# Optimization experiments

Measured on AMD Instinct MI355X. Metric: run time of the kernel, lower is better.

The kernel has to match this reference:

```python
import jax, jax.numpy as jnp
import numpy as np

N, E = 50000, 300000
IN, HID, OUT, HEADS = 768, 256, 128, 8
RELS = ("writes", "written_by", "cites")


def setup_inputs():
    ks = iter(jax.random.split(jax.random.key(0), 64))

    def nrm(shape, scale=1.0):
        return jax.random.normal(next(ks), shape, dtype=jnp.float32) * scale

    inp = {"x_paper": nrm((N, IN)), "x_author": nrm((N, IN))}
    for name in ("ei_writes", "ei_written_by", "ei_cites"):
        inp[name] = jax.random.randint(next(ks), (2, E), 0, N, dtype=jnp.int32)
    # layer 0: in=IN, out=HID, heads=HEADS
    s0 = 1.0 / np.sqrt(IN)
    inp["W0_paper"] = nrm((IN, HID), s0); inp["b0_paper"] = jnp.zeros((HID,), jnp.float32)
    inp["W0_author"] = nrm((IN, HID), s0); inp["b0_author"] = jnp.zeros((HID,), jnp.float32)
    D0 = HID // HEADS
    for rel in RELS:
        inp["a0s_" + rel] = nrm((HEADS, D0), 0.1)
        inp["a0d_" + rel] = nrm((HEADS, D0), 0.1)
    inp["Wk0"] = nrm((HID, HID), 1.0 / np.sqrt(HID)); inp["bk0"] = jnp.zeros((HID,), jnp.float32)
    inp["q0"] = nrm((HID,), 0.1)
    # layer 1 (last): in=HID, out=OUT, heads=1
    s1 = 1.0 / np.sqrt(HID)
    inp["W1_paper"] = nrm((HID, OUT), s1); inp["b1_paper"] = jnp.zeros((OUT,), jnp.float32)
    inp["W1_author"] = nrm((HID, OUT), s1); inp["b1_author"] = jnp.zeros((OUT,), jnp.float32)
    for rel in RELS:
        inp["a1s_" + rel] = nrm((1, OUT), 0.1)
        inp["a1d_" + rel] = nrm((1, OUT), 0.1)
    inp["Wk1"] = nrm((OUT, OUT), 1.0 / np.sqrt(OUT)); inp["bk1"] = jnp.zeros((OUT,), jnp.float32)
    inp["q1"] = nrm((OUT,), 0.1)
    return inp


def _han_layer(xs, proj, att, Wk, bk, q, edges, heads):
    # xs: {ntype: [N, in]}, proj: {ntype: (W, b)}, att: {rel: (a_src[H,D], a_dst[H,D])}
    C = q.shape[0]
    D = C // heads
    xh = {nt: (x @ proj[nt][0] + proj[nt][1]).reshape(-1, heads, D) for nt, x in xs.items()}
    outs = {nt: [] for nt in xs}
    for (st, rel, dt), ei in edges:
        a_s, a_d = att[rel]
        xsrc, xdst = xh[st], xh[dt]
        src, dst = ei[0], ei[1]
        n = xdst.shape[0]
        # GAT-style edge scores per head: [E, H]
        al = jax.nn.leaky_relu((xsrc * a_s).sum(-1)[src] + (xdst * a_d).sum(-1)[dst], 0.2)
        amax = jax.lax.stop_gradient(jax.ops.segment_max(al, dst, num_segments=n))
        ex = jnp.exp(al - amax[dst])
        alpha = ex / (jax.ops.segment_sum(ex, dst, num_segments=n)[dst] + 1e-16)
        msg = xsrc[src] * alpha[:, :, None]                      # [E, H, D]
        agg = jax.ops.segment_sum(msg, dst, num_segments=n)      # [n, H, D]
        outs[dt].append(jax.nn.relu(agg.reshape(n, C)))
    # semantic attention across metapaths (group)
    res = {}
    for nt, lst in outs.items():
        stk = jnp.stack(lst)                                     # [M, n, C]
        score = (q * jnp.tanh(stk @ Wk + bk).mean(axis=1)).sum(-1)
        w = jax.nn.softmax(score)                                # [M]
        res[nt] = jnp.einsum('m,mnc->nc', w, stk)
    return res


def reference(x_paper, x_author, W0_paper, b0_paper, W0_author, b0_author,
              a0s_writes, a0d_writes, a0s_written_by, a0d_written_by, a0s_cites, a0d_cites,
              Wk0, bk0, q0,
              W1_paper, b1_paper, W1_author, b1_author,
              a1s_writes, a1d_writes, a1s_written_by, a1d_written_by, a1s_cites, a1d_cites,
              Wk1, bk1, q1,
              ei_writes, ei_written_by, ei_cites):
    edges = [(("author", "writes", "paper"), ei_writes),
             (("paper", "written_by", "author"), ei_written_by),
             (("paper", "cites", "paper"), ei_cites)]
    h = _han_layer({"paper": x_paper, "author": x_author},
                   {"paper": (W0_paper, b0_paper), "author": (W0_author, b0_author)},
                   {"writes": (a0s_writes, a0d_writes),
                    "written_by": (a0s_written_by, a0d_written_by),
                    "cites": (a0s_cites, a0d_cites)},
                   Wk0, bk0, q0, edges, HEADS)
    h = {k: jax.nn.elu(v) for k, v in h.items()}
    h = _han_layer(h,
                   {"paper": (W1_paper, b1_paper), "author": (W1_author, b1_author)},
                   {"writes": (a1s_writes, a1d_writes),
                    "written_by": (a1s_written_by, a1d_written_by),
                    "cites": (a1s_cites, a1d_cites)},
                   Wk1, bk1, q1, edges, 1)

    def l2n(v):
        return v / jnp.maximum(jnp.linalg.norm(v, axis=1, keepdims=True), 1e-12)

    return (l2n(h["paper"]), l2n(h["author"]))
```

## Files before the change

kernel.cpp:

```cpp
#include <hip/hip_runtime.h>
#include <math.h>

#define NN 50000
#define NE 300000
#define DIN 768
#define DHID 256
#define DOUT 128
#define H0 8
#define D0 32
#define OFFST (NN + 4)

typedef __attribute__((ext_vector_type(8))) short bf16x8;
typedef __attribute__((ext_vector_type(8))) unsigned short u16x8;
typedef __attribute__((ext_vector_type(4))) float f32x4;

__device__ __forceinline__ unsigned short f2bf(float f) {
    unsigned u = __float_as_uint(f);
    unsigned r = (u + 0x7fffu + ((u >> 16) & 1u)) >> 16;
    return (unsigned short)r;
}
__device__ __forceinline__ float bf2f(unsigned short u) {
    return __uint_as_float(((unsigned)u) << 16);
}

__device__ __forceinline__ void gload16(const void* g, void* l) {
    __builtin_amdgcn_global_load_lds(
        (const __attribute__((address_space(1))) unsigned int*)g,
        (__attribute__((address_space(3))) unsigned int*)l, 16, 0, 0);
}

__device__ __forceinline__ void store_bf8(unsigned short* dst, float4 lo, float4 hi) {
    u16x8 o;
    o[0] = f2bf(lo.x); o[1] = f2bf(lo.y); o[2] = f2bf(lo.z); o[3] = f2bf(lo.w);
    o[4] = f2bf(hi.x); o[5] = f2bf(hi.y); o[6] = f2bf(hi.z); o[7] = f2bf(hi.w);
    *(u16x8*)dst = o;
}

__global__ void transconv3_kernel(const float* __restrict__ Wa, const float* __restrict__ Wb,
                                  const float* __restrict__ Wc,
                                  unsigned short* __restrict__ Ta, unsigned short* __restrict__ Tb,
                                  unsigned short* __restrict__ Tc,
                                  int Kab, int Nab, int Kc, int Ncc)
{
    int y = blockIdx.y;
    const float* W = (y == 0) ? Wa : ((y == 1) ? Wb : Wc);
    unsigned short* T = (y == 0) ? Ta : ((y == 1) ? Tb : Tc);
    int K = (y == 2) ? Kc : Kab;
    int Nc = (y == 2) ? Ncc : Nab;
    int gid = blockIdx.x * 256 + threadIdx.x;
    if (gid >= K * Nc) return;
    int k = gid / Nc, n = gid - k * Nc;
    T[(size_t)n * K + k] = f2bf(W[gid]);
}

__global__ __launch_bounds__(256) void gemm_l0_kernel(
    const float* __restrict__ A0, const float* __restrict__ A1,
    const unsigned short* __restrict__ Bt0, const unsigned short* __restrict__ Bt1,
    const float* __restrict__ bias0, const float* __restrict__ bias1,
    unsigned short* __restrict__ C0, unsigned short* __restrict__ C1)
{
    constexpr int K  = DIN;
    constexpr int Nc = DHID;
    constexpr int NT = K / 32;
    __shared__ __align__(16) unsigned short As[2][128 * 32];
    __shared__ __align__(16) unsigned short Bs[3][128 * 32];
    const int z = blockIdx.z;
    const float* A = z ? A1 : A0;
    const unsigned short* Bt = z ? Bt1 : Bt0;
    const float* bias = z ? bias1 : bias0;
    unsigned short* C = z ? C1 : C0;
    const int t = threadIdx.x;
    const int lane = t & 63, w = t >> 6;
    const int wr = w >> 1, wc = w & 1;
    const int bm = blockIdx.y * 128, bn = blockIdx.x * 128;

    f32x4 acc[4][4];
    #pragma unroll
    for (int m = 0; m < 4; ++m)
        #pragma unroll
        for (int n = 0; n < 4; ++n)
            acc[m][n] = (f32x4){0.f, 0.f, 0.f, 0.f};

    const int c0 = t, c1 = t + 256;
    const int row0 = c0 >> 2, row1 = c1 >> 2;
    const int g0 = (c0 & 3) ^ ((row0 >> 1) & 3);
    const int g1 = (c1 & 3) ^ ((row1 >> 1) & 3);
    int ar0 = bm + row0; if (ar0 >= NN) ar0 = NN - 1;
    int ar1 = bm + row1; if (ar1 >= NN) ar1 = NN - 1;
    const float* pA0 = A + (size_t)ar0 * K + g0 * 8;
    const float* pA1 = A + (size_t)ar1 * K + g1 * 8;
    const unsigned short* pB0 = Bt + (size_t)(bn + row0) * K + g0 * 8;
    const unsigned short* pB1 = Bt + (size_t)(bn + row1) * K + g1 * 8;

    const int rA = wr * 64 + (lane & 15);
    const int rB = wc * 64 + (lane & 15);
    const int gw = lane >> 4;

    float4 ra[2][4];
    {
        float4 t00 = *(const float4*)(pA0);
        float4 t01 = *(const float4*)(pA0 + 4);
        float4 t10 = *(const float4*)(pA1);
        float4 t11 = *(const float4*)(pA1 + 4);
        gload16(pB0, &Bs[0][c0 * 8]);
        gload16(pB1, &Bs[0][c1 * 8]);
        ra[1][0] = *(const float4*)(pA0 + 32);
        ra[1][1] = *(const float4*)(pA0 + 36);
        ra[1][2] = *(const float4*)(pA1 + 32);
        ra[1][3] = *(const float4*)(pA1 + 36);
        gload16(pB0 + 32, &Bs[1][c0 * 8]);
        gload16(pB1 + 32, &Bs[1][c1 * 8]);
        store_bf8(&As[0][c0 * 8], t00, t01);
        store_bf8(&As[0][c1 * 8], t10, t11);
    }
    asm volatile("s_waitcnt vmcnt(6) lgkmcnt(0)\n\ts_barrier" ::: "memory");

    #pragma unroll
    for (int ti = 0; ti < NT; ++ti) {
        const int rcv = ti & 1;
        const int con = rcv ^ 1;
        if (ti + 2 < NT) {
            const int nk = (ti + 2) * 32;
            ra[rcv][0] = *(const float4*)(pA0 + nk);
            ra[rcv][1] = *(const float4*)(pA0 + nk + 4);
            ra[rcv][2] = *(const float4*)(pA1 + nk);
            ra[rcv][3] = *(const float4*)(pA1 + nk + 4);
            gload16(pB0 + nk, &Bs[(ti + 2) % 3][c0 * 8]);
            gload16(pB1 + nk, &Bs[(ti + 2) % 3][c1 * 8]);
        }
        bf16x8 afr[4], bfr[4];
        #pragma unroll
        for (int m = 0; m < 4; ++m) {
            int r = rA + m * 16;
            afr[m] = *(const bf16x8*)&As[rcv][r * 32 + ((gw ^ ((r >> 1) & 3)) * 8)];
        }
        #pragma unroll
        for (int n = 0; n < 4; ++n) {
            int r = rB + n * 16;
            bfr[n] = *(const bf16x8*)&Bs[ti % 3][r * 32 + ((gw ^ ((r >> 1) & 3)) * 8)];
        }
        #pragma unroll
        for (int m = 0; m < 4; ++m)
            #pragma unroll
            for (int n = 0; n < 4; ++n)
                acc[m][n] = __builtin_amdgcn_mfma_f32_16x16x32_bf16(afr[m], bfr[n], acc[m][n], 0, 0, 0);
        if (ti + 1 < NT) {
            store_bf8(&As[con][c0 * 8], ra[con][0], ra[con][1]);
            store_bf8(&As[con][c1 * 8], ra[con][2], ra[con][3]);
            if (ti + 2 < NT) asm volatile("s_waitcnt vmcnt(6) lgkmcnt(0)\n\ts_barrier" ::: "memory");
            else             asm volatile("s_waitcnt vmcnt(0) lgkmcnt(0)\n\ts_barrier" ::: "memory");
        }
    }

    #pragma unroll
    for (int m = 0; m < 4; ++m) {
        #pragma unroll
        for (int j = 0; j < 4; ++j) {
            int row = bm + wr * 64 + m * 16 + (lane >> 4) * 4 + j;
            if (row >= NN) continue;
            #pragma unroll
            for (int n = 0; n < 4; ++n) {
                int col = bn + wc * 64 + n * 16 + (lane & 15);
                C[(size_t)row * Nc + col] = f2bf(acc[m][n][j] + bias[col]);
            }
        }
    }
}

__global__ __launch_bounds__(256) void gemm_bf16_kernel(
    const unsigned short* __restrict__ A0, const unsigned short* __restrict__ A1,
    const unsigned short* __restrict__ Bt0, const unsigned short* __restrict__ Bt1,
    const float* __restrict__ bias0, const float* __restrict__ bias1,
    unsigned short* __restrict__ C0, unsigned short* __restrict__ C1,
    int M, int K, int Nc)
{
    __shared__ __align__(16) unsigned short As[2][128 * 32];
    __shared__ __align__(16) unsigned short Bs[2][128 * 32];
    const int z = blockIdx.z;
    const unsigned short* A  = z ? A1  : A0;
    const unsigned short* Bt = z ? Bt1 : Bt0;
    const float* bias = z ? bias1 : bias0;
    unsigned short* C = z ? C1 : C0;
    const int t = threadIdx.x;
    const int lane = t & 63, w = t >> 6;
    const int wr = w >> 1, wc = w & 1;
    const int bm = blockIdx.y * 128, bn = blockIdx.x * 128;

    f32x4 acc[4][4];
    #pragma unroll
    for (int m = 0; m < 4; ++m)
        #pragma unroll
        for (int n = 0; n < 4; ++n)
            acc[m][n] = (f32x4){0.f, 0.f, 0.f, 0.f};

    const int c0 = w * 64 + lane, c1 = c0 + 256;
    const int row0 = c0 >> 2, row1 = c1 >> 2;
    const int g0 = (c0 & 3) ^ ((row0 >> 1) & 3);
    const int g1 = (c1 & 3) ^ ((row1 >> 1) & 3);
    const int ar0 = (bm + row0 < M) ? (bm + row0) : (M - 1);
    const int ar1 = (bm + row1 < M) ? (bm + row1) : (M - 1);
    const unsigned short* pA0 = A + (size_t)ar0 * K + g0 * 8;
    const unsigned short* pA1 = A + (size_t)ar1 * K + g1 * 8;
    const unsigned short* pB0 = Bt + (size_t)(bn + row0) * K + g0 * 8;
    const unsigned short* pB1 = Bt + (size_t)(bn + row1) * K + g1 * 8;

    const int rA = wr * 64 + (lane & 15);
    const int rB = wc * 64 + (lane & 15);
    const int gw = lane >> 4;
    const int nt = K >> 5;

    gload16(pA0, &As[0][c0 * 8]);
    gload16(pA1, &As[0][c1 * 8]);
    gload16(pB0, &Bs[0][c0 * 8]);
    gload16(pB1, &Bs[0][c1 * 8]);
    __syncthreads();
    for (int ti = 0; ti < nt; ++ti) {
        const int cur = ti & 1;
        if (ti + 1 < nt) {
            const int nk = (ti + 1) << 5;
            const int nb = cur ^ 1;
            gload16(pA0 + nk, &As[nb][c0 * 8]);
            gload16(pA1 + nk, &As[nb][c1 * 8]);
            gload16(pB0 + nk, &Bs[nb][c0 * 8]);
            gload16(pB1 + nk, &Bs[nb][c1 * 8]);
        }
        bf16x8 afr[4], bfr[4];
        #pragma unroll
        for (int m = 0; m < 4; ++m) {
            int r = rA + m * 16;
            afr[m] = *(const bf16x8*)&As[cur][r * 32 + ((gw ^ ((r >> 1) & 3)) * 8)];
        }
        #pragma unroll
        for (int n = 0; n < 4; ++n) {
            int r = rB + n * 16;
            bfr[n] = *(const bf16x8*)&Bs[cur][r * 32 + ((gw ^ ((r >> 1) & 3)) * 8)];
        }
        #pragma unroll
        for (int m = 0; m < 4; ++m)
            #pragma unroll
            for (int n = 0; n < 4; ++n)
                acc[m][n] = __builtin_amdgcn_mfma_f32_16x16x32_bf16(afr[m], bfr[n], acc[m][n], 0, 0, 0);
        __syncthreads();
    }
    #pragma unroll
    for (int m = 0; m < 4; ++m) {
        #pragma unroll
        for (int j = 0; j < 4; ++j) {
            int row = bm + wr * 64 + m * 16 + (lane >> 4) * 4 + j;
            if (row >= M) continue;
            #pragma unroll
            for (int n = 0; n < 4; ++n) {
                int col = bn + wc * 64 + n * 16 + (lane & 15);
                C[(size_t)row * Nc + col] = f2bf(acc[m][n][j] + bias[col]);
            }
        }
    }
}

__global__ __launch_bounds__(256) void sem_bf16_kernel(
    const unsigned short* __restrict__ A, const unsigned short* __restrict__ Bt,
    const float* __restrict__ bk, float* __restrict__ partial,
    int M, int K, int Nc)
{
    __shared__ __align__(16) unsigned short As[2][128 * 32];
    __shared__ __align__(16) unsigned short Bs[2][128 * 32];
    __shared__ float red[128];
    const int t = threadIdx.x;
    const int lane = t & 63, w = t >> 6;
    const int wr = w >> 1, wc = w & 1;
    const int bm = blockIdx.y * 128, bn = blockIdx.x * 128;

    f32x4 acc[4][4];
    #pragma unroll
    for (int m = 0; m < 4; ++m)
        #pragma unroll
        for (int n = 0; n < 4; ++n)
            acc[m][n] = (f32x4){0.f, 0.f, 0.f, 0.f};

    const int c0 = w * 64 + lane, c1 = c0 + 256;
    const int row0 = c0 >> 2, row1 = c1 >> 2;
    const int g0 = (c0 & 3) ^ ((row0 >> 1) & 3);
    const int g1 = (c1 & 3) ^ ((row1 >> 1) & 3);
    const int ar0 = (bm + row0 < M) ? (bm + row0) : (M - 1);
    const int ar1 = (bm + row1 < M) ? (bm + row1) : (M - 1);
    const unsigned short* pA0 = A + (size_t)ar0 * K + g0 * 8;
    const unsigned short* pA1 = A + (size_t)ar1 * K + g1 * 8;
    const unsigned short* pB0 = Bt + (size_t)(bn + row0) * K + g0 * 8;
    const unsigned short* pB1 = Bt + (size_t)(bn + row1) * K + g1 * 8;

    const int rA = wr * 64 + (lane & 15);
    const int rB = wc * 64 + (lane & 15);
    const int gw = lane >> 4;
    const int nt = K >> 5;

    gload16(pA0, &As[0][c0 * 8]);
    gload16(pA1, &As[0][c1 * 8]);
    gload16(pB0, &Bs[0][c0 * 8]);
    gload16(pB1, &Bs[0][c1 * 8]);
    __syncthreads();
    for (int ti = 0; ti < nt; ++ti) {
        const int cur = ti & 1;
        if (ti + 1 < nt) {
            const int nk = (ti + 1) << 5;
            const int nb = cur ^ 1;
            gload16(pA0 + nk, &As[nb][c0 * 8]);
            gload16(pA1 + nk, &As[nb][c1 * 8]);
            gload16(pB0 + nk, &Bs[nb][c0 * 8]);
            gload16(pB1 + nk, &Bs[nb][c1 * 8]);
        }
        bf16x8 afr[4], bfr[4];
        #pragma unroll
        for (int m = 0; m < 4; ++m) {
            int r = rA + m * 16;
            afr[m] = *(const bf16x8*)&As[cur][r * 32 + ((gw ^ ((r >> 1) & 3)) * 8)];
        }
        #pragma unroll
        for (int n = 0; n < 4; ++n) {
            int r = rB + n * 16;
            bfr[n] = *(const bf16x8*)&Bs[cur][r * 32 + ((gw ^ ((r >> 1) & 3)) * 8)];
        }
        #pragma unroll
        for (int m = 0; m < 4; ++m)
            #pragma unroll
            for (int n = 0; n < 4; ++n)
                acc[m][n] = __builtin_amdgcn_mfma_f32_16x16x32_bf16(afr[m], bfr[n], acc[m][n], 0, 0, 0);
        __syncthreads();
    }
    if (t < 128) red[t] = 0.f;
    __syncthreads();
    #pragma unroll
    for (int n = 0; n < 4; ++n) {
        int lcol = wc * 64 + n * 16 + (lane & 15);
        float b = bk[bn + lcol];
        float s = 0.f;
        #pragma unroll
        for (int m = 0; m < 4; ++m) {
            #pragma unroll
            for (int j = 0; j < 4; ++j) {
                int row = bm + wr * 64 + m * 16 + (lane >> 4) * 4 + j;
                if (row < M) s += tanhf(acc[m][n][j] + b);
            }
        }
        atomicAdd(&red[lcol], s);
    }
    __syncthreads();
    if (t < 128) atomicAdd(&partial[bn + t], red[t]);
}

__global__ void hist3_kernel(const int* __restrict__ d0, const int* __restrict__ d1,
                             const int* __restrict__ d2, int* __restrict__ deg3)
{
    int gid = blockIdx.x * 256 + threadIdx.x;
    if (gid >= 3 * NE) return;
    int rel = gid / NE, e = gid - rel * NE;
    const int* dst = (rel == 0) ? d0 : ((rel == 1) ? d1 : d2);
    atomicAdd(&deg3[rel * NN + dst[e]], 1);
}

__global__ void block_sum3_kernel(const int* __restrict__ deg3, int* __restrict__ bsum3)
{
    __shared__ int buf[256];
    int rel = blockIdx.y;
    int i = blockIdx.x * 256 + threadIdx.x;
    buf[threadIdx.x] = (i < NN) ? deg3[rel * NN + i] : 0;
    __syncthreads();
    for (int s = 128; s > 0; s >>= 1) {
        if (threadIdx.x < s) buf[threadIdx.x] += buf[threadIdx.x + s];
        __syncthreads();
    }
    if (threadIdx.x == 0) bsum3[rel * 256 + blockIdx.x] = buf[0];
}

__global__ void scan_bsum3_kernel(const int* __restrict__ bsum3, int* __restrict__ boff3, int nb)
{
    __shared__ int buf[256];
    int rel = blockIdx.y;
    int tid = threadIdx.x;
    int v = (tid < nb) ? bsum3[rel * 256 + tid] : 0;
    buf[tid] = v;
    __syncthreads();
    for (int off = 1; off < 256; off <<= 1) {
        int t = (tid >= off) ? buf[tid - off] : 0;
        __syncthreads();
        buf[tid] += t;
        __syncthreads();
    }
    if (tid < nb) boff3[rel * 256 + tid] = buf[tid] - v;
}

__global__ void scan_final3_kernel(const int* __restrict__ deg3, const int* __restrict__ boff3,
                                   int* __restrict__ offs3)
{
    __shared__ int buf[256];
    int rel = blockIdx.y;
    int tid = threadIdx.x, b = blockIdx.x;
    int i = b * 256 + tid;
    int v = (i < NN) ? deg3[rel * NN + i] : 0;
    buf[tid] = v;
    __syncthreads();
    for (int off = 1; off < 256; off <<= 1) {
        int t = (tid >= off) ? buf[tid - off] : 0;
        __syncthreads();
        buf[tid] += t;
        __syncthreads();
    }
    int* offs = offs3 + rel * OFFST;
    if (i < NN) offs[i] = boff3[rel * 256 + b] + buf[tid] - v;
    if (i == NN - 1) offs[NN] = boff3[rel * 256 + b] + buf[tid];
}

__global__ void place3_kernel(const int* __restrict__ s0, const int* __restrict__ s1,
                              const int* __restrict__ s2,
                              const int* __restrict__ offs3, int* __restrict__ cnt3,
                              int* __restrict__ esrc3)
{
    int rel = blockIdx.y;
    int e = blockIdx.x * 256 + threadIdx.x;
    if (e >= NE) return;
    const int* srcdst = (rel == 0) ? s0 : ((rel == 1) ? s1 : s2);
    int src = srcdst[e];
    int d = srcdst[NE + e];
    int p = offs3[rel * OFFST + d] + atomicAdd(&cnt3[rel * NN + d], 1);
    esrc3[rel * NE + p] = src;
}

__global__ void scores_L0_kernel(
    const unsigned short* __restrict__ xp, const unsigned short* __restrict__ xa,
    const float* __restrict__ a_dw, const float* __restrict__ a_swb,
    const float* __restrict__ a_sc, const float* __restrict__ a_dc,
    const float* __restrict__ a_sw, const float* __restrict__ a_dwb,
    float* __restrict__ sW_dst, float* __restrict__ sWB_src,
    float* __restrict__ sC_src, float* __restrict__ sC_dst,
    float* __restrict__ sW_src, float* __restrict__ sWB_dst)
{
    int gid = blockIdx.x * 256 + threadIdx.x;
    int half = NN * H0;
    if (gid >= 2 * half) return;
    if (gid < half) {
        int node = gid >> 3, h = gid & 7;
        const unsigned short* xr = xp + (size_t)node * DHID + h * D0;
        float xv[D0];
        #pragma unroll
        for (int j = 0; j < 4; ++j) {
            u16x8 v = ((const u16x8*)xr)[j];
            #pragma unroll
            for (int k = 0; k < 8; ++k) xv[j * 8 + k] = bf2f(v[k]);
        }
        const float* p0 = a_dw  + h * D0;
        const float* p1 = a_swb + h * D0;
        const float* p2 = a_sc  + h * D0;
        const float* p3 = a_dc  + h * D0;
        float d0 = 0.f, d1 = 0.f, d2 = 0.f, d3 = 0.f;
        #pragma unroll
        for (int k = 0; k < D0; ++k) {
            float x = xv[k];
            d0 += x * p0[k]; d1 += x * p1[k]; d2 += x * p2[k]; d3 += x * p3[k];
        }
        sW_dst[gid] = d0; sWB_src[gid] = d1; sC_src[gid] = d2; sC_dst[gid] = d3;
    } else {
        int g = gid - half;
        int node = g >> 3, h = g & 7;
        const unsigned short* xr = xa + (size_t)node * DHID + h * D0;
        float xv[D0];
        #pragma unroll
        for (int j = 0; j < 4; ++j) {
            u16x8 v = ((const u16x8*)xr)[j];
            #pragma unroll
            for (int k = 0; k < 8; ++k) xv[j * 8 + k] = bf2f(v[k]);
        }
        const float* p0 = a_sw  + h * D0;
        const float* p1 = a_dwb + h * D0;
        float d0 = 0.f, d1 = 0.f;
        #pragma unroll
        for (int k = 0; k < D0; ++k) {
            float x = xv[k];
            d0 += x * p0[k]; d1 += x * p1[k];
        }
        sW_src[g] = d0; sWB_dst[g] = d1;
    }
}

__global__ void scores_L1_kernel(
    const unsigned short* __restrict__ xp, const unsigned short* __restrict__ xa,
    const float* __restrict__ a_dw, const float* __restrict__ a_swb,
    const float* __restrict__ a_sc, const float* __restrict__ a_dc,
    const float* __restrict__ a_sw, const float* __restrict__ a_dwb,
    float* __restrict__ sW_dst, float* __restrict__ sWB_src,
    float* __restrict__ sC_src, float* __restrict__ sC_dst,
    float* __restrict__ sW_src, float* __restrict__ sWB_dst)
{
    int gid = blockIdx.x * 256 + threadIdx.x;
    if (gid >= 2 * NN) return;
    if (gid < NN) {
        const unsigned short* xr = xp + (size_t)gid * DOUT;
        float d0 = 0.f, d1 = 0.f, d2 = 0.f, d3 = 0.f;
        for (int j = 0; j < DOUT / 8; ++j) {
            u16x8 v = ((const u16x8*)xr)[j];
            #pragma unroll
            for (int k = 0; k < 8; ++k) {
                float x = bf2f(v[k]);
                int c = j * 8 + k;
                d0 += x * a_dw[c]; d1 += x * a_swb[c]; d2 += x * a_sc[c]; d3 += x * a_dc[c];
            }
        }
        sW_dst[gid] = d0; sWB_src[gid] = d1; sC_src[gid] = d2; sC_dst[gid] = d3;
    } else {
        int g = gid - NN;
        const unsigned short* xr = xa + (size_t)g * DOUT;
        float d0 = 0.f, d1 = 0.f;
        for (int j = 0; j < DOUT / 8; ++j) {
            u16x8 v = ((const u16x8*)xr)[j];
            #pragma unroll
            for (int k = 0; k < 8; ++k) {
                float x = bf2f(v[k]);
                int c = j * 8 + k;
                d0 += x * a_sw[c]; d1 += x * a_dwb[c];
            }
        }
        sW_src[g] = d0; sWB_dst[g] = d1;
    }
}

__global__ void seg_alpha3_kernel(
    const int* __restrict__ offs3, const int* __restrict__ esrc3,
    const float* __restrict__ ss0, const float* __restrict__ ss1, const float* __restrict__ ss2,
    const float* __restrict__ sd0, const float* __restrict__ sd1, const float* __restrict__ sd2,
    float* __restrict__ alpha3, int H)
{
    int rel = blockIdx.y;
    const int* offs = offs3 + rel * OFFST;
    const int* esrc = esrc3 + rel * NE;
    const float* ssrc = (rel == 0) ? ss0 : ((rel == 1) ? ss1 : ss2);
    const float* sdst = (rel == 0) ? sd0 : ((rel == 1) ? sd1 : sd2);
    float* alpha = alpha3 + (size_t)rel * NE * H0;
    int gid = blockIdx.x * 256 + threadIdx.x;
    if (gid >= NN * H) return;
    int d = gid / H, h = gid - d * H;
    int beg = offs[d], end = offs[d + 1];
    float sd = sdst[gid];
    float m = -INFINITY, den = 0.f;
    for (int i = beg; i < end; ++i) {
        int s = esrc[i];
        float v = ssrc[s * H + h] + sd;
        v = (v >= 0.f) ? v : 0.2f * v;
        if (v > m) { den = den * expf(m - v) + 1.f; m = v; }
        else       den += expf(v - m);
    }
    float inv = 1.f / (den + 1e-16f);
    for (int i = beg; i < end; ++i) {
        int s = esrc[i];
        float v = ssrc[s * H + h] + sd;
        v = (v >= 0.f) ? v : 0.2f * v;
        alpha[(size_t)i * H + h] = expf(v - m) * inv;
    }
}

template<int CPL, int HH, int DSH>
__global__ __launch_bounds__(256) void gather3_kernel(
    const int* __restrict__ offs3, const int* __restrict__ esrc3,
    const float* __restrict__ alpha3,
    const unsigned short* __restrict__ x0, const unsigned short* __restrict__ x1,
    const unsigned short* __restrict__ x2,
    unsigned short* __restrict__ o0, unsigned short* __restrict__ o1,
    unsigned short* __restrict__ o2, int C)
{
    int rel = blockIdx.y;
    const int* offs = offs3 + rel * OFFST;
    const int* esrc = esrc3 + rel * NE;
    const float* alpha = alpha3 + (size_t)rel * NE * H0;
    const unsigned short* x = (rel == 0) ? x0 : ((rel == 1) ? x1 : x2);
    unsigned short* outp = (rel == 0) ? o0 : ((rel == 1) ? o1 : o2);

    int wid = threadIdx.x >> 6, lane = threadIdx.x & 63;
    int d = blockIdx.x * 4 + wid;
    int c0 = lane * CPL;
    int h = c0 >> DSH;
    int beg = offs[d], end = offs[d + 1];
    float acc0 = 0.f, acc1 = 0.f, acc2 = 0.f, acc3 = 0.f;
    int n = end - beg;
    if (n > 0) {
        int sA = esrc[beg];
        float aA = alpha[(size_t)beg * HH + h];
        int sB = sA; float aB = 0.f;
        if (n > 1) { sB = esrc[beg + 1]; aB = alpha[(size_t)(beg + 1) * HH + h]; }
        if (CPL == 4) {
            ushort4 xc = *(const ushort4*)(x + (size_t)sA * C + c0);
            for (int i = beg; i < end; ++i) {
                ushort4 xn = xc;
                if (i + 1 < end) xn = *(const ushort4*)(x + (size_t)sB * C + c0);
                int sN = sB; float aN = 0.f;
                if (i + 2 < end) { sN = esrc[i + 2]; aN = alpha[(size_t)(i + 2) * HH + h]; }
                acc0 += aA * bf2f(xc.x); acc1 += aA * bf2f(xc.y);
                acc2 += aA * bf2f(xc.z); acc3 += aA * bf2f(xc.w);
                xc = xn; aA = aB; sB = sN; aB = aN;
            }
        } else {
            ushort2 xc = *(const ushort2*)(x + (size_t)sA * C + c0);
            for (int i = beg; i < end; ++i) {
                ushort2 xn = xc;
                if (i + 1 < end) xn = *(const ushort2*)(x + (size_t)sB * C + c0);
                int sN = sB; float aN = 0.f;
                if (i + 2 < end) { sN = esrc[i + 2]; aN = alpha[(size_t)(i + 2) * HH + h]; }
                acc0 += aA * bf2f(xc.x); acc1 += aA * bf2f(xc.y);
                xc = xn; aA = aB; sB = sN; aB = aN;
            }
        }
    }
    unsigned short* op = outp + (size_t)d * C + c0;
    if (CPL == 4) {
        ushort4 st;
        st.x = f2bf(fmaxf(acc0, 0.f)); st.y = f2bf(fmaxf(acc1, 0.f));
        st.z = f2bf(fmaxf(acc2, 0.f)); st.w = f2bf(fmaxf(acc3, 0.f));
        *(ushort4*)op = st;
    } else {
        ushort2 st;
        st.x = f2bf(fmaxf(acc0, 0.f)); st.y = f2bf(fmaxf(acc1, 0.f));
        *(ushort2*)op = st;
    }
}

__global__ void sem_weights_kernel(const float* __restrict__ partial, const float* __restrict__ q,
                                   float* __restrict__ w, int C, int n)
{
    if (threadIdx.x != 0 || blockIdx.x != 0) return;
    float inv = 1.f / (float)n;
    float s0 = 0.f, s1 = 0.f;
    for (int c = 0; c < C; ++c) {
        s0 += q[c] * partial[c] * inv;
        s1 += q[c] * partial[C + c] * inv;
    }
    float m = fmaxf(s0, s1);
    float e0 = expf(s0 - m), e1 = expf(s1 - m);
    float den = e0 + e1;
    w[0] = e0 / den;
    w[1] = e1 / den;
}

__global__ void combine2_bf16_kernel(const unsigned short* __restrict__ a,
                                     const unsigned short* __restrict__ b,
                                     const float* __restrict__ w, unsigned short* __restrict__ out,
                                     int n8)
{
    int i = blockIdx.x * 256 + threadIdx.x;
    if (i >= n8) return;
    float w0 = w[0], w1 = w[1];
    u16x8 va = ((const u16x8*)a)[i];
    u16x8 vb = ((const u16x8*)b)[i];
    u16x8 o;
    #pragma unroll
    for (int j = 0; j < 8; ++j) o[j] = f2bf(w0 * bf2f(va[j]) + w1 * bf2f(vb[j]));
    ((u16x8*)out)[i] = o;
}

__global__ __launch_bounds__(128) void final_norm_kernel(
    const unsigned short* __restrict__ aggW, const unsigned short* __restrict__ aggC,
    const unsigned short* __restrict__ aggB, const float* __restrict__ w,
    float* __restrict__ out)
{
    __shared__ float red[128];
    int row = blockIdx.x;
    int c = threadIdx.x;
    float v;
    if (row < NN) {
        size_t i = (size_t)row * DOUT + c;
        v = w[0] * bf2f(aggW[i]) + w[1] * bf2f(aggC[i]);
    } else {
        size_t i = (size_t)(row - NN) * DOUT + c;
        v = bf2f(aggB[i]);
    }
    red[c] = v * v;
    __syncthreads();
    for (int s = 64; s > 0; s >>= 1) {
        if (c < s) red[c] += red[c + s];
        __syncthreads();
    }
    float norm = sqrtf(red[0]);
    out[(size_t)row * DOUT + c] = v / fmaxf(norm, 1e-12f);
}

extern "C" void kernel_launch(void* const* d_in, const int* in_sizes, int n_in,
                              void* d_out, int out_size, void* d_ws, size_t ws_size,
                              hipStream_t stream)
{
    const float* x_paper   = (const float*)d_in[0];
    const float* x_author  = (const float*)d_in[1];
    const int*   ei_writes = (const int*)d_in[2];
    const int*   ei_wb     = (const int*)d_in[3];
    const int*   ei_cites  = (const int*)d_in[4];
    const float* W0p = (const float*)d_in[5];  const float* b0p = (const float*)d_in[6];
    const float* W0a = (const float*)d_in[7];  const float* b0a = (const float*)d_in[8];
    const float* a0s_w  = (const float*)d_in[9];  const float* a0d_w  = (const float*)d_in[10];
    const float* a0s_wb = (const float*)d_in[11]; const float* a0d_wb = (const float*)d_in[12];
    const float* a0s_c  = (const float*)d_in[13]; const float* a0d_c  = (const float*)d_in[14];
    const float* Wk0 = (const float*)d_in[15]; const float* bk0 = (const float*)d_in[16];
    const float* q0  = (const float*)d_in[17];
    const float* W1p = (const float*)d_in[18]; const float* b1p = (const float*)d_in[19];
    const float* W1a = (const float*)d_in[20]; const float* b1a = (const float*)d_in[21];
    const float* a1s_w  = (const float*)d_in[22]; const float* a1d_w  = (const float*)d_in[23];
    const float* a1s_wb = (const float*)d_in[24]; const float* a1d_wb = (const float*)d_in[25];
    const float* a1s_c  = (const float*)d_in[26]; const float* a1d_c  = (const float*)d_in[27];
    const float* Wk1 = (const float*)d_in[28]; const float* bk1 = (const float*)d_in[29];
    const float* q1  = (const float*)d_in[30];

    float* out = (float*)d_out;

    const size_t NH = (size_t)NN * DHID;
    const size_t NI = (size_t)NN * DIN;
    const size_t NO = (size_t)NN * DOUT;
    const size_t NH2 = NH * 2;
    const size_t NI2 = NI * 2;
    const size_t NO2 = NO * 2;

    char* base = (char*)d_ws;
    unsigned short* xbhP = (unsigned short*)(base + 0);
    unsigned short* xbhA = (unsigned short*)(base + NH2);
    unsigned short* aggW = (unsigned short*)(base + 2 * NH2);
    unsigned short* aggC = (unsigned short*)(base + 3 * NH2);
    unsigned short* aggB = (unsigned short*)(base + 4 * NH2);
    unsigned short* hbP  = (unsigned short*)(base + 0);
    unsigned short* hbA  = aggB;
    unsigned short* x1Pb = (unsigned short*)(base + NH2);
    unsigned short* x1Ab = (unsigned short*)(base + NH2 + NO2);
    unsigned short* agg1W = (unsigned short*)(base + 2 * NH2 + NI2);
    unsigned short* agg1C = (unsigned short*)(base + 2 * NH2 + NI2 + NO2);
    unsigned short* agg1B = (unsigned short*)(base + 2 * NH2 + NI2 + 2 * NO2);

    float* sW_src  = (float*)(base + 204800000);
    float* sW_dst  = sW_src  + NN * H0;
    float* sWB_src = sW_dst  + NN * H0;
    float* sWB_dst = sWB_src + NN * H0;
    float* sC_src  = sWB_dst + NN * H0;
    float* sC_dst  = sC_src  + NN * H0;
    float* alpha3  = (float*)(base + 214400000);
    int* ip     = (int*)(base + 243200000);
    int* offs3  = ip;  ip += 3 * OFFST;
    int* esrc3  = ip;  ip += 3 * NE;
    int* deg3   = ip;  ip += 3 * NN;
    int* bsum3  = ip;  ip += 3 * 256;
    int* boff3  = ip;  ip += 3 * 256;
    unsigned short* wt0p = (unsigned short*)ip;
    unsigned short* wt0a = wt0p + (size_t)DHID * DIN;
    unsigned short* wkt  = wt0a + (size_t)DHID * DIN;
    unsigned short* wt1p = wt0p;
    unsigned short* wt1a = wt1p + (size_t)DOUT * DHID;
    float* tsum = (float*)(wkt + (size_t)DHID * DHID);
    float* wsem = tsum + 512;

    const int NB = (NN + 255) / 256;

    hipMemsetAsync(deg3, 0, 3 * NN * sizeof(int), stream);
    hist3_kernel<<<(3 * NE + 255) / 256, 256, 0, stream>>>(ei_writes + NE, ei_wb + NE, ei_cites + NE, deg3);
    block_sum3_kernel<<<dim3(NB, 3), 256, 0, stream>>>(deg3, bsum3);
    scan_bsum3_kernel<<<dim3(1, 3), 256, 0, stream>>>(bsum3, boff3, NB);
    scan_final3_kernel<<<dim3(NB, 3), 256, 0, stream>>>(deg3, boff3, offs3);
    hipMemsetAsync(deg3, 0, 3 * NN * sizeof(int), stream);
    place3_kernel<<<dim3((NE + 255) / 256, 3), 256, 0, stream>>>(ei_writes, ei_wb, ei_cites, offs3, deg3, esrc3);

    hipMemsetAsync(tsum, 0, 512 * sizeof(float), stream);
    transconv3_kernel<<<dim3((DIN * DHID + 255) / 256, 3), 256, 0, stream>>>(
        W0p, W0a, Wk0, wt0p, wt0a, wkt, DIN, DHID, DHID, DHID);

    dim3 g0(DHID / 128, (NN + 127) / 128, 2);
    gemm_l0_kernel<<<g0, 256, 0, stream>>>(x_paper, x_author, wt0p, wt0a, b0p, b0a, xbhP, xbhA);

    scores_L0_kernel<<<(2 * NN * H0 + 255) / 256, 256, 0, stream>>>(
        xbhP, xbhA, a0d_w, a0s_wb, a0s_c, a0d_c, a0s_w, a0d_wb,
        sW_dst, sWB_src, sC_src, sC_dst, sW_src, sWB_dst);
    dim3 ga0((NN * H0 + 255) / 256, 3);
    seg_alpha3_kernel<<<ga0, 256, 0, stream>>>(
        offs3, esrc3, sW_src, sWB_src, sC_src, sW_dst, sWB_dst, sC_dst, alpha3, H0);
    dim3 gg0(NN / 4, 3);
    gather3_kernel<4, H0, 5><<<gg0, 256, 0, stream>>>(
        offs3, esrc3, alpha3, xbhA, xbhP, xbhP, aggW, aggB, aggC, DHID);

    dim3 gs0(DHID / 128, (NN + 127) / 128);
    sem_bf16_kernel<<<gs0, 256, 0, stream>>>(aggW, wkt, bk0, tsum,        NN, DHID, DHID);
    sem_bf16_kernel<<<gs0, 256, 0, stream>>>(aggC, wkt, bk0, tsum + DHID, NN, DHID, DHID);
    sem_weights_kernel<<<1, 64, 0, stream>>>(tsum, q0, wsem, DHID, NN);

    combine2_bf16_kernel<<<(int)((NH / 8 + 255) / 256), 256, 0, stream>>>(aggW, aggC, wsem, hbP, (int)(NH / 8));

    transconv3_kernel<<<dim3((DHID * DOUT + 255) / 256, 3), 256, 0, stream>>>(
        W1p, W1a, Wk1, wt1p, wt1a, wkt, DHID, DOUT, DOUT, DOUT);

    dim3 g1(DOUT / 128, (NN + 127) / 128, 2);
    gemm_bf16_kernel<<<g1, 256, 0, stream>>>(hbP, hbA, wt1p, wt1a, b1p, b1a, x1Pb, x1Ab, NN, DHID, DOUT);

    hipMemsetAsync(tsum, 0, 2 * DOUT * sizeof(float), stream);

    scores_L1_kernel<<<(2 * NN + 255) / 256, 256, 0, stream>>>(
        x1Pb, x1Ab, a1d_w, a1s_wb, a1s_c, a1d_c, a1s_w, a1d_wb,
        sW_dst, sWB_src, sC_src, sC_dst, sW_src, sWB_dst);
    dim3 ga1((NN + 255) / 256, 3);
    seg_alpha3_kernel<<<ga1, 256, 0, stream>>>(
        offs3, esrc3, sW_src, sWB_src, sC_src, sW_dst, sWB_dst, sC_dst, alpha3, 1);
    dim3 gg1(NN / 4, 3);
    gather3_kernel<2, 1, 7><<<gg1, 256, 0, stream>>>(
        offs3, esrc3, alpha3, x1Ab, x1Pb, x1Pb, agg1W, agg1B, agg1C, DOUT);

    dim3 gs1(DOUT / 128, (NN + 127) / 128);
    sem_bf16_kernel<<<gs1, 256, 0, stream>>>(agg1W, wkt, bk1, tsum,        NN, DOUT, DOUT);
    sem_bf16_kernel<<<gs1, 256, 0, stream>>>(agg1C, wkt, bk1, tsum + DOUT, NN, DOUT, DOUT);
    sem_weights_kernel<<<1, 64, 0, stream>>>(tsum, q1, wsem, DOUT, NN);

    final_norm_kernel<<<2 * NN, 128, 0, stream>>>(agg1W, agg1C, agg1B, wsem, out);
}
```

Baseline: 750.1 us.

## Widen layer-0 GEMM tile to full 256 columns and batch semantic GEMMs

The layer-0 projection GEMM now uses 512-thread blocks covering all 256 output columns per 128-row tile. Each fp32 A row is loaded and converted to bf16 once instead of once per column block, which halves A traffic. The B pipeline changes from triple to double buffering with adjusted waitcnts. The two semantic-attention GEMM launches per layer are merged into a single launch using blockIdx.z, cutting launch overhead. The larger block and LDS footprint may lower occupancy.

```diff
diff --git a/kernel.cpp b/kernel.cpp
--- a/kernel.cpp
+++ b/kernel.cpp
@@ -53,7 +53,7 @@
     T[(size_t)n * K + k] = f2bf(W[gid]);
 }
 
-__global__ __launch_bounds__(256) void gemm_l0_kernel(
+__global__ __launch_bounds__(512) void gemm_l0_kernel(
     const float* __restrict__ A0, const float* __restrict__ A1,
     const unsigned short* __restrict__ Bt0, const unsigned short* __restrict__ Bt1,
     const float* __restrict__ bias0, const float* __restrict__ bias1,
@@ -63,16 +63,16 @@
     constexpr int Nc = DHID;
     constexpr int NT = K / 32;
     __shared__ __align__(16) unsigned short As[2][128 * 32];
-    __shared__ __align__(16) unsigned short Bs[3][128 * 32];
-    const int z = blockIdx.z;
+    __shared__ __align__(16) unsigned short Bs[2][256 * 32];
+    const int z = blockIdx.y;
     const float* A = z ? A1 : A0;
     const unsigned short* Bt = z ? Bt1 : Bt0;
     const float* bias = z ? bias1 : bias0;
     unsigned short* C = z ? C1 : C0;
     const int t = threadIdx.x;
     const int lane = t & 63, w = t >> 6;
-    const int wr = w >> 1, wc = w & 1;
-    const int bm = blockIdx.y * 128, bn = blockIdx.x * 128;
+    const int wr = w >> 2, wc = w & 3;
+    const int bm = blockIdx.x * 128;
 
     f32x4 acc[4][4];
     #pragma unroll
@@ -81,63 +81,60 @@
         for (int n = 0; n < 4; ++n)
             acc[m][n] = (f32x4){0.f, 0.f, 0.f, 0.f};
 
-    const int c0 = t, c1 = t + 256;
-    const int row0 = c0 >> 2, row1 = c1 >> 2;
-    const int g0 = (c0 & 3) ^ ((row0 >> 1) & 3);
-    const int g1 = (c1 & 3) ^ ((row1 >> 1) & 3);
-    int ar0 = bm + row0; if (ar0 >= NN) ar0 = NN - 1;
-    int ar1 = bm + row1; if (ar1 >= NN) ar1 = NN - 1;
-    const float* pA0 = A + (size_t)ar0 * K + g0 * 8;
-    const float* pA1 = A + (size_t)ar1 * K + g1 * 8;
-    const unsigned short* pB0 = Bt + (size_t)(bn + row0) * K + g0 * 8;
-    const unsigned short* pB1 = Bt + (size_t)(bn + row1) * K + g1 * 8;
+    const int arow = t >> 2;
+    const int ags = (t & 3) ^ ((arow >> 1) & 3);
+    int ar = bm + arow; if (ar >= NN) ar = NN - 1;
+    const float* pA = A + (size_t)ar * K + ags * 8;
+    const int b0row = t >> 2;
+    const int bg0 = (t & 3) ^ ((b0row >> 1) & 3);
+    const unsigned short* pB0 = Bt + (size_t)b0row * K + bg0 * 8;
+    const int c1i = t + 512;
+    const int b1row = c1i >> 2;
+    const int bg1 = (c1i & 3) ^ ((b1row >> 1) & 3);
+    const unsigned short* pB1 = Bt + (size_t)b1row * K + bg1 * 8;
 
     const int rA = wr * 64 + (lane & 15);
     const int rB = wc * 64 + (lane & 15);
     const int gw = lane >> 4;
 
-    float4 ra[2][4];
+    float4 ra[2][2];
     {
-        float4 t00 = *(const float4*)(pA0);
-        float4 t01 = *(const float4*)(pA0 + 4);
-        float4 t10 = *(const float4*)(pA1);
-        float4 t11 = *(const float4*)(pA1 + 4);
-        gload16(pB0, &Bs[0][c0 * 8]);
-        gload16(pB1, &Bs[0][c1 * 8]);
-        ra[1][0] = *(const float4*)(pA0 + 32);
-        ra[1][1] = *(const float4*)(pA0 + 36);
-        ra[1][2] = *(const float4*)(pA1 + 32);
-        ra[1][3] = *(const float4*)(pA1 + 36);
-        gload16(pB0 + 32, &Bs[1][c0 * 8]);
-        gload16(pB1 + 32, &Bs[1][c1 * 8]);
-        store_bf8(&As[0][c0 * 8], t00, t01);
-        store_bf8(&As[0][c1 * 8], t10, t11);
-    }
-    asm volatile("s_waitcnt vmcnt(6) lgkmcnt(0)\n\ts_barrier" ::: "memory");
+        float4 t0 = *(const float4*)(pA);
+        float4 t1 = *(const float4*)(pA + 4);
+        gload16(pB0, &Bs[0][(size_t)t * 8]);
+        gload16(pB1, &Bs[0][(size_t)c1i * 8]);
+        ra[1][0] = *(const float4*)(pA + 32);
+        ra[1][1] = *(const float4*)(pA + 36);
+        gload16(pB0 + 32, &Bs[1][(size_t)t * 8]);
+        gload16(pB1 + 32, &Bs[1][(size_t)c1i * 8]);
+        store_bf8(&As[0][(size_t)t * 8], t0, t1);
+    }
+    asm volatile("s_waitcnt vmcnt(4) lgkmcnt(0)\n\ts_barrier" ::: "memory");
 
     #pragma unroll
     for (int ti = 0; ti < NT; ++ti) {
-        const int rcv = ti & 1;
-        const int con = rcv ^ 1;
+        const int cur = ti & 1;
+        const int nxt = cur ^ 1;
+        if (ti + 1 < NT) {
+            const int nk = (ti + 1) * 32;
+            gload16(pB0 + nk, &Bs[nxt][(size_t)t * 8]);
+            gload16(pB1 + nk, &Bs[nxt][(size_t)c1i * 8]);
+        }
         if (ti + 2 < NT) {
             const int nk = (ti + 2) * 32;
-            ra[rcv][0] = *(const float4*)(pA0 + nk);
-            ra[rcv][1] = *(const float4*)(pA0 + nk + 4);
-            ra[rcv][2] = *(const float4*)(pA1 + nk);
-            ra[rcv][3] = *(const float4*)(pA1 + nk + 4);
-            gload16(pB0 + nk, &Bs[(ti + 2) % 3][c0 * 8]);
-            gload16(pB1 + nk, &Bs[(ti + 2) % 3][c1 * 8]);
+            ra[cur][0] = *(const float4*)(pA + nk);
+            ra[cur][1] = *(const float4*)(pA + nk + 4);
         }
         bf16x8 afr[4], bfr[4];
         #pragma unroll
         for (int m = 0; m < 4; ++m) {
             int r = rA + m * 16;
-            afr[m] = *(const bf16x8*)&As[rcv][r * 32 + ((gw ^ ((r >> 1) & 3)) * 8)];
+            afr[m] = *(const bf16x8*)&As[cur][r * 32 + ((gw ^ ((r >> 1) & 3)) * 8)];
         }
         #pragma unroll
         for (int n = 0; n < 4; ++n) {
             int r = rB + n * 16;
-            bfr[n] = *(const bf16x8*)&Bs[ti % 3][r * 32 + ((gw ^ ((r >> 1) & 3)) * 8)];
+            bfr[n] = *(const bf16x8*)&Bs[cur][r * 32 + ((gw ^ ((r >> 1) & 3)) * 8)];
         }
         #pragma unroll
         for (int m = 0; m < 4; ++m)
@@ -145,9 +142,8 @@
             for (int n = 0; n < 4; ++n)
                 acc[m][n] = __builtin_amdgcn_mfma_f32_16x16x32_bf16(afr[m], bfr[n], acc[m][n], 0, 0, 0);
         if (ti + 1 < NT) {
-            store_bf8(&As[con][c0 * 8], ra[con][0], ra[con][1]);
-            store_bf8(&As[con][c1 * 8], ra[con][2], ra[con][3]);
-            if (ti + 2 < NT) asm volatile("s_waitcnt vmcnt(6) lgkmcnt(0)\n\ts_barrier" ::: "memory");
+            store_bf8(&As[nxt][(size_t)t * 8], ra[nxt][0], ra[nxt][1]);
+            if (ti + 2 < NT) asm volatile("s_waitcnt vmcnt(2) lgkmcnt(0)\n\ts_barrier" ::: "memory");
             else             asm volatile("s_waitcnt vmcnt(0) lgkmcnt(0)\n\ts_barrier" ::: "memory");
         }
     }
@@ -160,7 +156,7 @@
             if (row >= NN) continue;
             #pragma unroll
             for (int n = 0; n < 4; ++n) {
-                int col = bn + wc * 64 + n * 16 + (lane & 15);
+                int col = wc * 64 + n * 16 + (lane & 15);
                 C[(size_t)row * Nc + col] = f2bf(acc[m][n][j] + bias[col]);
             }
         }
@@ -257,14 +253,18 @@
     }
 }
 
-__global__ __launch_bounds__(256) void sem_bf16_kernel(
-    const unsigned short* __restrict__ A, const unsigned short* __restrict__ Bt,
-    const float* __restrict__ bk, float* __restrict__ partial,
+__global__ __launch_bounds__(256) void sem2_bf16_kernel(
+    const unsigned short* __restrict__ Aa, const unsigned short* __restrict__ Ab,
+    const unsigned short* __restrict__ Bt,
+    const float* __restrict__ bk, float* __restrict__ partial0,
     int M, int K, int Nc)
 {
     __shared__ __align__(16) unsigned short As[2][128 * 32];
     __shared__ __align__(16) unsigned short Bs[2][128 * 32];
     __shared__ float red[128];
+    const int z = blockIdx.z;
+    const unsigned short* A = z ? Ab : Aa;
+    float* partial = partial0 + z * Nc;
     const int t = threadIdx.x;
     const int lane = t & 63, w = t >> 6;
     const int wr = w >> 1, wc = w & 1;
@@ -760,8 +760,8 @@
     transconv3_kernel<<<dim3((DIN * DHID + 255) / 256, 3), 256, 0, stream>>>(
         W0p, W0a, Wk0, wt0p, wt0a, wkt, DIN, DHID, DHID, DHID);
 
-    dim3 g0(DHID / 128, (NN + 127) / 128, 2);
-    gemm_l0_kernel<<<g0, 256, 0, stream>>>(x_paper, x_author, wt0p, wt0a, b0p, b0a, xbhP, xbhA);
+    dim3 g0((NN + 127) / 128, 2);
+    gemm_l0_kernel<<<g0, 512, 0, stream>>>(x_paper, x_author, wt0p, wt0a, b0p, b0a, xbhP, xbhA);
 
     scores_L0_kernel<<<(2 * NN * H0 + 255) / 256, 256, 0, stream>>>(
         xbhP, xbhA, a0d_w, a0s_wb, a0s_c, a0d_c, a0s_w, a0d_wb,
@@ -773,9 +773,8 @@
     gather3_kernel<4, H0, 5><<<gg0, 256, 0, stream>>>(
         offs3, esrc3, alpha3, xbhA, xbhP, xbhP, aggW, aggB, aggC, DHID);
 
-    dim3 gs0(DHID / 128, (NN + 127) / 128);
-    sem_bf16_kernel<<<gs0, 256, 0, stream>>>(aggW, wkt, bk0, tsum,        NN, DHID, DHID);
-    sem_bf16_kernel<<<gs0, 256, 0, stream>>>(aggC, wkt, bk0, tsum + DHID, NN, DHID, DHID);
+    dim3 gs0(DHID / 128, (NN + 127) / 128, 2);
+    sem2_bf16_kernel<<<gs0, 256, 0, stream>>>(aggW, aggC, wkt, bk0, tsum, NN, DHID, DHID);
     sem_weights_kernel<<<1, 64, 0, stream>>>(tsum, q0, wsem, DHID, NN);
 
     combine2_bf16_kernel<<<(int)((NH / 8 + 255) / 256), 256, 0, stream>>>(aggW, aggC, wsem, hbP, (int)(NH / 8));
@@ -798,9 +797,8 @@
     gather3_kernel<2, 1, 7><<<gg1, 256, 0, stream>>>(
         offs3, esrc3, alpha3, x1Ab, x1Pb, x1Pb, agg1W, agg1B, agg1C, DOUT);
 
-    dim3 gs1(DOUT / 128, (NN + 127) / 128);
-    sem_bf16_kernel<<<gs1, 256, 0, stream>>>(agg1W, wkt, bk1, tsum,        NN, DOUT, DOUT);
-    sem_bf16_kernel<<<gs1, 256, 0, stream>>>(agg1C, wkt, bk1, tsum + DOUT, NN, DOUT, DOUT);
+    dim3 gs1(DOUT / 128, (NN + 127) / 128, 2);
+    sem2_bf16_kernel<<<gs1, 256, 0, stream>>>(agg1W, agg1C, wkt, bk1, tsum, NN, DOUT, DOUT);
     sem_weights_kernel<<<1, 64, 0, stream>>>(tsum, q1, wsem, DOUT, NN);
 
     final_norm_kernel<<<2 * NN, 128, 0, stream>>>(agg1W, agg1C, agg1B, wsem, out);
```

New measurement: 728.0 us. -3.0%, faster.
